# Performance work log

Hardware: AMD Instinct MI355X
Metric: run time of the kernel (lower is better)

## Reference

```python
import jax, jax.numpy as jnp
from jax import lax
import numpy as np

B, N, G, K = 4, 1024, 128, 32
D_MODEL, DEPTH, CLS = 384, 12, 40
D_INNER, D_STATE, D_CONV, DT_RANK = 768, 16, 4, 24
EPS = 1e-5
BN_SCALE = 1.0 / float(np.sqrt(1.0 + EPS))  # eval BN, running_mean=0, running_var=1


def layernorm(x, w, b):
    mu = x.mean(-1, keepdims=True)
    var = ((x - mu) ** 2).mean(-1, keepdims=True)
    return (x - mu) * lax.rsqrt(var + EPS) * w + b


def bn_eval(x, g, b):
    return x * (g * BN_SCALE) + b


def fps(xyz, n):
    Bb, Nn, _ = xyz.shape
    first = jnp.zeros((Bb,), jnp.int32)

    def step(carry, _):
        dmin, last = carry
        p = jnp.take_along_axis(xyz, last[:, None, None], axis=1)  # B,1,3
        dmin = jnp.minimum(dmin, jnp.sum((xyz - p) ** 2, -1))
        nxt = jnp.argmax(dmin, -1).astype(jnp.int32)
        return (dmin, nxt), nxt

    _, rest = lax.scan(step, (jnp.full((Bb, Nn), 1e10, xyz.dtype), first), None, length=n - 1)
    return jnp.concatenate([first[None, :], rest], 0).T  # B,G


def group_points(xyz):
    idx = fps(xyz, G)
    center = jnp.take_along_axis(xyz, idx[:, :, None], axis=1)            # B,G,3
    d2 = jnp.sum((center[:, :, None, :] - xyz[:, None, :, :]) ** 2, -1)   # B,G,N
    _, knn = lax.top_k(-d2, K)                                            # B,G,K
    nb = jax.vmap(lambda p, i: p[i])(xyz, knn)                            # B,G,K,3
    return nb - center[:, :, None, :], center


def encoder(pg, w1, b1, g1, bb1, w2, b2, w3, b3, g2, bb2, w4, b4):
    Bb, Gg, Kk, _ = pg.shape
    f = pg.reshape(Bb * Gg, Kk, 3)
    f = jax.nn.relu(bn_eval(f @ w1.T + b1, g1, bb1))                      # BG,K,128
    f = f @ w2.T + b2                                                     # BG,K,256
    fg = f.max(1, keepdims=True)
    f = jnp.concatenate([jnp.broadcast_to(fg, f.shape), f], -1)           # BG,K,512
    f = jax.nn.relu(bn_eval(f @ w3.T + b3, g2, bb2))
    f = f @ w4.T + b4
    return f.max(1).reshape(Bb, Gg, -1)                                   # B,G,C


def mamba_mixer(x, ipw, cw, cb, xpw, dpw, dpb, A_log, Dp, opw):
    L = x.shape[1]
    xz = x @ ipw.T                                                        # B,L,2*Di
    u, z = jnp.split(xz, 2, -1)
    up = jnp.pad(u, ((0, 0), (D_CONV - 1, 0), (0, 0)))                    # causal depthwise conv
    u = sum(up[:, k:k + L, :] * cw[:, k] for k in range(D_CONV)) + cb
    u = jax.nn.silu(u)
    xdb = u @ xpw.T
    dt, Bm, Cm = jnp.split(xdb, [DT_RANK, DT_RANK + D_STATE], -1)
    dt = jax.nn.softplus(dt @ dpw.T + dpb)                                # B,L,Di
    A = -jnp.exp(A_log)                                                   # Di,Ds

    def step(h, inp):
        dt_t, B_t, C_t, u_t = inp
        h = jnp.exp(dt_t[:, :, None] * A) * h + (dt_t * u_t)[:, :, None] * B_t[:, None, :]
        return h, jnp.einsum('bds,bs->bd', h, C_t)

    h0 = jnp.zeros((x.shape[0], D_INNER, D_STATE), x.dtype)
    _, ys = lax.scan(step, h0, (dt.swapaxes(0, 1), Bm.swapaxes(0, 1), Cm.swapaxes(0, 1), u.swapaxes(0, 1)))
    y = ys.swapaxes(0, 1) + u * Dp
    return (y * jax.nn.silu(z)) @ opw.T


def forward(pts, enc_w1, enc_b1, enc_bn1_g, enc_bn1_b, enc_w2, enc_b2, enc_w3, enc_b3,
            enc_bn2_g, enc_bn2_b, enc_w4, enc_b4, pos_w1, pos_b1, pos_w2, pos_b2,
            ln_w, ln_b, in_proj_w, conv_w, conv_b, x_proj_w, dt_proj_w, dt_proj_b,
            A_log, D_param, out_proj_w, normf_w, normf_b, norm_w, norm_b,
            head_w1, head_b1, head_bn1_g, head_bn1_b, head_w2, head_b2,
            head_bn2_g, head_bn2_b, head_w3, head_b3):
    nb, center = group_points(pts)
    tok = encoder(nb, enc_w1, enc_b1, enc_bn1_g, enc_bn1_b, enc_w2, enc_b2,
                  enc_w3, enc_b3, enc_bn2_g, enc_bn2_b, enc_w4, enc_b4)    # B,G,384
    pos = jax.nn.gelu(center @ pos_w1.T + pos_b1, approximate=False) @ pos_w2.T + pos_b2

    # PointMamba token reordering: sort by center x, y, z and concatenate -> L = 3G
    toks, poss = [], []
    for ax in range(3):
        o = jnp.argsort(center[:, :, ax], axis=-1)[:, :, None]
        toks.append(jnp.take_along_axis(tok, o, axis=1))
        poss.append(jnp.take_along_axis(pos, o, axis=1))
    tok = jnp.concatenate(toks, 1)
    pos = jnp.concatenate(poss, 1)

    h = tok + pos
    res = jnp.zeros_like(h)

    def layer_step(carry, p):
        h, res = carry
        lnw, lnb, ipw, cw, cb, xpw, dpw, dpb, Al, Dp, opw = p
        res = h + res
        x = layernorm(res, lnw, lnb)
        h = mamba_mixer(x, ipw, cw, cb, xpw, dpw, dpb, Al, Dp, opw)
        return (h, res), None

    (h, res), _ = lax.scan(layer_step, (h, res),
                           (ln_w, ln_b, in_proj_w, conv_w, conv_b, x_proj_w,
                            dt_proj_w, dt_proj_b, A_log, D_param, out_proj_w))
    x = layernorm(h + res, normf_w, normf_b)   # MixerModel.norm_f
    x = layernorm(x, norm_w, norm_b)           # PointMamba.norm
    feat = x.mean(1)                           # B,384
    h1 = jax.nn.relu(bn_eval(feat @ head_w1.T + head_b1, head_bn1_g, head_bn1_b))
    h2 = jax.nn.relu(bn_eval(h1 @ head_w2.T + head_b2, head_bn2_g, head_bn2_b))
    return h2 @ head_w3.T + head_b3            # B,CLS


def setup_inputs():
    key = jax.random.key(0)
    ks = iter(jax.random.split(key, 64))

    def rn(shape, s=0.02):
        return jax.random.normal(next(ks), shape, jnp.float32) * s

    inp = dict(
        pts=jax.random.normal(next(ks), (B, N, 3), jnp.float32),
        enc_w1=rn((128, 3), 0.1), enc_b1=jnp.zeros((128,)),
        enc_bn1_g=jnp.ones((128,)), enc_bn1_b=jnp.zeros((128,)),
        enc_w2=rn((256, 128), 0.05), enc_b2=jnp.zeros((256,)),
        enc_w3=rn((512, 512), 0.05), enc_b3=jnp.zeros((512,)),
        enc_bn2_g=jnp.ones((512,)), enc_bn2_b=jnp.zeros((512,)),
        enc_w4=rn((D_MODEL, 512), 0.05), enc_b4=jnp.zeros((D_MODEL,)),
        pos_w1=rn((128, 3), 0.1), pos_b1=jnp.zeros((128,)),
        pos_w2=rn((D_MODEL, 128), 0.05), pos_b2=jnp.zeros((D_MODEL,)),
        ln_w=jnp.ones((DEPTH, D_MODEL)), ln_b=jnp.zeros((DEPTH, D_MODEL)),
        in_proj_w=rn((DEPTH, 2 * D_INNER, D_MODEL)),
        conv_w=rn((DEPTH, D_INNER, D_CONV), 0.2), conv_b=jnp.zeros((DEPTH, D_INNER)),
        x_proj_w=rn((DEPTH, DT_RANK + 2 * D_STATE, D_INNER)),
        dt_proj_w=rn((DEPTH, D_INNER, DT_RANK), 0.1),
        dt_proj_b=jnp.full((DEPTH, D_INNER), -4.6, jnp.float32),
        A_log=jnp.broadcast_to(jnp.log(jnp.arange(1, D_STATE + 1, dtype=jnp.float32)),
                               (DEPTH, D_INNER, D_STATE)).copy(),
        D_param=jnp.ones((DEPTH, D_INNER)),
        out_proj_w=rn((DEPTH, D_MODEL, D_INNER)),
        normf_w=jnp.ones((D_MODEL,)), normf_b=jnp.zeros((D_MODEL,)),
        norm_w=jnp.ones((D_MODEL,)), norm_b=jnp.zeros((D_MODEL,)),
        head_w1=rn((256, D_MODEL), 0.05), head_b1=jnp.zeros((256,)),
        head_bn1_g=jnp.ones((256,)), head_bn1_b=jnp.zeros((256,)),
        head_w2=rn((256, 256), 0.05), head_b2=jnp.zeros((256,)),
        head_bn2_g=jnp.ones((256,)), head_bn2_b=jnp.zeros((256,)),
        head_w3=rn((CLS, 256), 0.05), head_b3=jnp.zeros((CLS,)),
    )
    return inp


def reference(pts, enc_w1, enc_b1, enc_bn1_g, enc_bn1_b, enc_w2, enc_b2, enc_w3, enc_b3,
              enc_bn2_g, enc_bn2_b, enc_w4, enc_b4, pos_w1, pos_b1, pos_w2, pos_b2,
              ln_w, ln_b, in_proj_w, conv_w, conv_b, x_proj_w, dt_proj_w, dt_proj_b,
              A_log, D_param, out_proj_w, normf_w, normf_b, norm_w, norm_b,
              head_w1, head_b1, head_bn1_g, head_bn1_b, head_w2, head_b2,
              head_bn2_g, head_bn2_b, head_w3, head_b3):
    return forward(pts, enc_w1, enc_b1, enc_bn1_g, enc_bn1_b, enc_w2, enc_b2, enc_w3, enc_b3,
                   enc_bn2_g, enc_bn2_b, enc_w4, enc_b4, pos_w1, pos_b1, pos_w2, pos_b2,
                   ln_w, ln_b, in_proj_w, conv_w, conv_b, x_proj_w, dt_proj_w, dt_proj_b,
                   A_log, D_param, out_proj_w, normf_w, normf_b, norm_w, norm_b,
                   head_w1, head_b1, head_bn1_g, head_bn1_b, head_w2, head_b2,
                   head_bn2_g, head_bn2_b, head_w3, head_b3)
```

## Files before the change

### kernel.cpp

```cpp
#include <hip/hip_runtime.h>
#include <hip/hip_bf16.h>

using bf16 = __hip_bfloat16;
using short8  = __attribute__((ext_vector_type(8))) short;
using floatx4 = __attribute__((ext_vector_type(4))) float;
using ull = unsigned long long;

constexpr int Bn = 4, Np = 1024, Gn = 128, Kn = 32;
constexpr int DM = 384, DEPTH = 12, CLSn = 40;
constexpr int DI = 768, DSt = 16, DTR = 24;
constexpr int Ln = 384;
constexpr int NCH = 12, CHS = 32;
constexpr int XDBS = 1536*56;
constexpr float EPSf = 1e-5f;
constexpr float BNS = 0.99999500003749968752f;
constexpr float LOG2E = 1.4426950408889634f;

static __device__ __forceinline__ short f2bf(float f){
  bf16 h = __float2bfloat16(f);
  return *reinterpret_cast<short*>(&h);
}
static __device__ __forceinline__ float fsig(float x){ return 1.f/(1.f + __expf(-x)); }
static __device__ __forceinline__ float fsoftplus(float x){
  return fmaxf(x, 0.f) + __logf(1.f + __expf(-fabsf(x)));
}

template<int CTRL>
static __device__ __forceinline__ int dppmov(int x){
  return __builtin_amdgcn_update_dpp(0, x, CTRL, 0xF, 0xF, true);
}
static __device__ __forceinline__ ull redmax64(ull key){
  #define RSTEP(CTRL) { \
    int hi = (int)(unsigned)(key >> 32), lo = (int)(unsigned)key; \
    int h2 = dppmov<CTRL>(hi), l2 = dppmov<CTRL>(lo); \
    ull k2 = ((ull)(unsigned)h2 << 32) | (unsigned)l2; \
    if (k2 > key) key = k2; }
  RSTEP(0x111) RSTEP(0x112) RSTEP(0x114) RSTEP(0x118) RSTEP(0x142) RSTEP(0x143)
  #undef RSTEP
  return key;
}
static __device__ __forceinline__ int redmax32(int k){
  #define MSTEP(CTRL) { int o = dppmov<CTRL>(k); k = max(k, o); }
  MSTEP(0x111) MSTEP(0x112) MSTEP(0x114) MSTEP(0x118) MSTEP(0x142) MSTEP(0x143)
  #undef MSTEP
  return k;
}

__global__ __launch_bounds__(64) void fps_kernel(const float* __restrict__ pts,
                                                 float* __restrict__ center){
  int b = blockIdx.x, t = threadIdx.x;
  __shared__ float xs[1024], ys[1024], zs[1024];
  const float* p = pts + (size_t)b * Np * 3;
  float X[16], Y[16], Z[16], D[16];
  #pragma unroll
  for (int i = 0; i < 16; ++i){
    int n = t + 64*i;
    float a = p[n*3+0], c = p[n*3+1], e = p[n*3+2];
    X[i] = a; Y[i] = c; Z[i] = e;
    xs[n] = a; ys[n] = c; zs[n] = e;
    D[i] = 1e10f;
  }
  __syncthreads();
  float px = xs[0], py = ys[0], pz = zs[0];
  if (t == 0){
    center[(size_t)(b*Gn)*3+0] = px;
    center[(size_t)(b*Gn)*3+1] = py;
    center[(size_t)(b*Gn)*3+2] = pz;
  }
  for (int it = 1; it < Gn; ++it){
    float dm[16];
    #pragma unroll
    for (int i = 0; i < 16; ++i){
      float dx = __fsub_rn(X[i], px);
      float dy = __fsub_rn(Y[i], py);
      float dz = __fsub_rn(Z[i], pz);
      float d  = __fadd_rn(__fadd_rn(__fmul_rn(dx,dx), __fmul_rn(dy,dy)), __fmul_rn(dz,dz));
      float v  = fminf(D[i], d); D[i] = v; dm[i] = v;
    }
    float m2[8], m4[4];
    #pragma unroll
    for (int i = 0; i < 8; ++i) m2[i] = fmaxf(dm[2*i], dm[2*i+1]);
    #pragma unroll
    for (int i = 0; i < 4; ++i) m4[i] = fmaxf(m2[2*i], m2[2*i+1]);
    float vloc = fmaxf(fmaxf(m4[0], m4[1]), fmaxf(m4[2], m4[3]));
    int kv = redmax32(__float_as_int(vloc));
    float M = __int_as_float(__builtin_amdgcn_readlane(kv, 63));
    int e8[8], e4[4];
    #pragma unroll
    for (int i = 0; i < 8; ++i){
      int ka = (dm[2*i]   == M) ? (2047 - (t + 64*(2*i)))   : 0;
      int kb = (dm[2*i+1] == M) ? (2047 - (t + 64*(2*i+1))) : 0;
      e8[i] = max(ka, kb);
    }
    #pragma unroll
    for (int i = 0; i < 4; ++i) e4[i] = max(e8[2*i], e8[2*i+1]);
    int eloc = max(max(e4[0], e4[1]), max(e4[2], e4[3]));
    eloc = redmax32(eloc);
    int wn = 2047 - __builtin_amdgcn_readlane(eloc, 63);
    wn = min(max(wn, 0), Np-1);
    px = xs[wn]; py = ys[wn]; pz = zs[wn];
    if (t == 0){
      center[(size_t)(b*Gn+it)*3+0] = px;
      center[(size_t)(b*Gn+it)*3+1] = py;
      center[(size_t)(b*Gn+it)*3+2] = pz;
    }
  }
}

__global__ __launch_bounds__(256) void knn_kernel(const float* __restrict__ pts,
                                                  const float* __restrict__ center,
                                                  float* __restrict__ nb){
  int gid = blockIdx.x; int b = gid >> 7;
  __shared__ float d2[1024];
  __shared__ float rv[4]; __shared__ int ri[4];
  int t = threadIdx.x;
  float cx = center[(size_t)gid*3+0], cy = center[(size_t)gid*3+1], cz = center[(size_t)gid*3+2];
  const float* p = pts + (size_t)b * Np * 3;
  for (int n = t; n < Np; n += 256){
    float dx = __fsub_rn(cx, p[n*3+0]);
    float dy = __fsub_rn(cy, p[n*3+1]);
    float dz = __fsub_rn(cz, p[n*3+2]);
    d2[n] = __fadd_rn(__fadd_rn(__fmul_rn(dx,dx), __fmul_rn(dy,dy)), __fmul_rn(dz,dz));
  }
  __syncthreads();
  for (int kk = 0; kk < Kn; ++kk){
    float v = 3e38f; int idx = 0;
    for (int n = t; n < Np; n += 256){
      float d = d2[n];
      if (d < v || (d == v && n < idx)){ v = d; idx = n; }
    }
    ull key = ((ull)(unsigned)(~__float_as_uint(v)) << 32) | (unsigned)(Np-1 - idx);
    key = redmax64(key);
    if ((t & 63) == 63){
      rv[t>>6] = __uint_as_float(~(unsigned)(key >> 32));
      ri[t>>6] = Np-1 - (int)(unsigned)(key & 0xFFFFFFFFu);
    }
    __syncthreads();
    if (t == 0){
      float bv = rv[0]; int bi = ri[0];
      for (int w = 1; w < 4; ++w){
        if (rv[w] < bv || (rv[w] == bv && ri[w] < bi)){ bv = rv[w]; bi = ri[w]; }
      }
      bi = min(max(bi, 0), Np-1);
      nb[((size_t)gid*Kn+kk)*3+0] = __fsub_rn(p[bi*3+0], cx);
      nb[((size_t)gid*Kn+kk)*3+1] = __fsub_rn(p[bi*3+1], cy);
      nb[((size_t)gid*Kn+kk)*3+2] = __fsub_rn(p[bi*3+2], cz);
      d2[bi] = 3e38f;
    }
    __syncthreads();
  }
}

__global__ __launch_bounds__(256) void cvt_all(const float* __restrict__ s0,
    const float* __restrict__ s1, const float* __restrict__ s2,
    const float* __restrict__ s3, const float* __restrict__ s4,
    const float* __restrict__ s5, bf16* __restrict__ dst){
  long i = ((long)blockIdx.x*256 + threadIdx.x)*4;
  if (i >= 11624448L) return;
  const float* s; long off;
  if      (i <  7077888L){ s = s0; off = 0L; }
  else if (i < 10616832L){ s = s1; off =  7077888L; }
  else if (i < 11132928L){ s = s2; off = 10616832L; }
  else if (i < 11165696L){ s = s3; off = 11132928L; }
  else if (i < 11427840L){ s = s4; off = 11165696L; }
  else                   { s = s5; off = 11427840L; }
  float4 v = *(const float4*)(s + (i - off));
  short* o = (short*)dst + i;
  o[0] = f2bf(v.x); o[1] = f2bf(v.y); o[2] = f2bf(v.z); o[3] = f2bf(v.w);
}

template<typename AT, typename WT, int ACT, int MODE>
__global__ __launch_bounds__(256) void gemm_mfma(const AT* __restrict__ A, int lda,
                                                 const WT* __restrict__ W,
                                                 const float* __restrict__ bias,
                                                 const float* __restrict__ gz,
                                                 const float* __restrict__ bbp,
                                                 float* __restrict__ C, int ldc,
                                                 int M, int N, int K){
  __shared__ __align__(16) short As[64*40];
  __shared__ __align__(16) short Ws[64*40];
  int bm = blockIdx.x * 64, bn = blockIdx.y * 64;
  int t = threadIdx.x;
  int row = t >> 2;
  int kseg = (t & 3) * 8;
  int w = t >> 6, lane = t & 63, m16 = lane & 15, q = lane >> 4;
  floatx4 acc[4] = {};
  for (int k0 = 0; k0 < K; k0 += 32){
    {
      const float* Ar = (const float*)A + (size_t)(bm + row)*lda;
      short* dst = &As[row*40 + kseg];
      #pragma unroll
      for (int j = 0; j < 8; ++j){
        int k = k0 + kseg + j;
        dst[j] = (k < K) ? f2bf(Ar[k]) : (short)0;
      }
    }
    {
      int n = bn + row;
      short* dst = &Ws[row*40 + kseg];
      #pragma unroll
      for (int j = 0; j < 8; ++j){
        int k = k0 + kseg + j;
        dst[j] = (n < N && k < K) ? f2bf(((const float*)W)[(size_t)n*K + k]) : (short)0;
      }
    }
    __syncthreads();
    short8 af = *(const short8*)&As[(w*16 + m16)*40 + q*8];
    #pragma unroll
    for (int j = 0; j < 4; ++j){
      short8 bfr = *(const short8*)&Ws[(j*16 + m16)*40 + q*8];
      acc[j] = __builtin_amdgcn_mfma_f32_16x16x32_bf16(af, bfr, acc[j], 0, 0, 0);
    }
    __syncthreads();
  }
  #pragma unroll
  for (int j = 0; j < 4; ++j){
    int n = bn + j*16 + m16;
    if (n < N){
      float bv = bias ? bias[n] : 0.f;
      float gv = 0.f, bbv = 0.f;
      if (ACT == 1){ gv = gz[n] * BNS; bbv = bbp[n]; }
      #pragma unroll
      for (int r = 0; r < 4; ++r){
        int m = bm + w*16 + q*4 + r;
        float v = acc[j][r] + bv;
        if (ACT == 1){ v = v * gv + bbv; v = fmaxf(v, 0.f); }
        C[(size_t)m*ldc + n] = v;
      }
    }
  }
}

template<typename AT, typename WT, int ACT, int MODE>
__global__ __launch_bounds__(256) void gemm_mfma64(const AT* __restrict__ A, int lda,
                                                   const WT* __restrict__ W,
                                                   const float* __restrict__ bias,
                                                   const float* __restrict__ gz,
                                                   const float* __restrict__ bbp,
                                                   float* __restrict__ C, int ldc,
                                                   int M, int N, int K){
  __shared__ __align__(16) short As[64*72];
  __shared__ __align__(16) short Ws[64*72];
  int bm = blockIdx.x * 64, bn = blockIdx.y * 64;
  int t = threadIdx.x;
  int row = t >> 2;
  int kseg = (t & 3) * 16;
  int w = t >> 6, lane = t & 63, m16 = lane & 15, q = lane >> 4;
  floatx4 acc[4] = {};
  for (int k0 = 0; k0 < K; k0 += 64){
    if constexpr (MODE == 1){
      const float* Yr = (const float*)A + (size_t)(bm + row)*lda + k0 + kseg;
      const float* Zr = gz + (size_t)(bm + row)*1536 + 768 + k0 + kseg;
      float y[16], z[16];
      #pragma unroll
      for (int j = 0; j < 4; ++j){
        *(float4*)&y[j*4] = *(const float4*)(Yr + j*4);
        *(float4*)&z[j*4] = *(const float4*)(Zr + j*4);
      }
      short* dst = &As[row*72 + kseg];
      #pragma unroll
      for (int jj = 0; jj < 16; ++jj) dst[jj] = f2bf(y[jj] * (z[jj] * fsig(z[jj])));
    } else if constexpr (sizeof(AT) == 2){
      const short* Ar = (const short*)A + (size_t)(bm + row)*lda + k0 + kseg;
      *(short8*)&As[row*72 + kseg]     = *(const short8*)Ar;
      *(short8*)&As[row*72 + kseg + 8] = *(const short8*)(Ar + 8);
    } else {
      const float* Ar = (const float*)A + (size_t)(bm + row)*lda + k0 + kseg;
      float a[16];
      #pragma unroll
      for (int j = 0; j < 4; ++j) *(float4*)&a[j*4] = *(const float4*)(Ar + j*4);
      short* dst = &As[row*72 + kseg];
      #pragma unroll
      for (int jj = 0; jj < 16; ++jj) dst[jj] = f2bf(a[jj]);
    }
    {
      int n = bn + row;
      if constexpr (sizeof(WT) == 2){
        short8 v0, v1;
        #pragma unroll
        for (int j = 0; j < 8; ++j){ v0[j] = 0; v1[j] = 0; }
        if (n < N){
          const short* Wr = (const short*)W + (size_t)n*K + k0 + kseg;
          v0 = *(const short8*)Wr;
          v1 = *(const short8*)(Wr + 8);
        }
        *(short8*)&Ws[row*72 + kseg]     = v0;
        *(short8*)&Ws[row*72 + kseg + 8] = v1;
      } else {
        short* dst = &Ws[row*72 + kseg];
        if (n < N){
          const float* Wr = (const float*)W + (size_t)n*K + k0 + kseg;
          float wv[16];
          #pragma unroll
          for (int j = 0; j < 4; ++j) *(float4*)&wv[j*4] = *(const float4*)(Wr + j*4);
          #pragma unroll
          for (int jj = 0; jj < 16; ++jj) dst[jj] = f2bf(wv[jj]);
        } else {
          #pragma unroll
          for (int jj = 0; jj < 16; ++jj) dst[jj] = 0;
        }
      }
    }
    __syncthreads();
    short8 af0 = *(const short8*)&As[(w*16 + m16)*72 + q*8];
    short8 af1 = *(const short8*)&As[(w*16 + m16)*72 + 32 + q*8];
    #pragma unroll
    for (int j = 0; j < 4; ++j){
      short8 b0 = *(const short8*)&Ws[(j*16 + m16)*72 + q*8];
      acc[j] = __builtin_amdgcn_mfma_f32_16x16x32_bf16(af0, b0, acc[j], 0, 0, 0);
      short8 b1 = *(const short8*)&Ws[(j*16 + m16)*72 + 32 + q*8];
      acc[j] = __builtin_amdgcn_mfma_f32_16x16x32_bf16(af1, b1, acc[j], 0, 0, 0);
    }
    __syncthreads();
  }
  #pragma unroll
  for (int j = 0; j < 4; ++j){
    int n = bn + j*16 + m16;
    if (n < N){
      float bv = bias ? bias[n] : 0.f;
      float gv = 0.f, bbv = 0.f;
      if (ACT == 1){ gv = gz[n] * BNS; bbv = bbp[n]; }
      #pragma unroll
      for (int r = 0; r < 4; ++r){
        int m = bm + w*16 + q*4 + r;
        float v = acc[j][r] + bv;
        if (ACT == 1){ v = v * gv + bbv; v = fmaxf(v, 0.f); }
        C[(size_t)m*ldc + n] = v;
      }
    }
  }
}

template<typename WT>
__global__ __launch_bounds__(256) void xproj_kernel(const float* __restrict__ xz,
                                                    const WT* __restrict__ W,
                                                    const float* __restrict__ cw,
                                                    const float* __restrict__ cb,
                                                    float* __restrict__ xdbp,
                                                    int KB){
  __shared__ __align__(16) short As[64*72];
  __shared__ __align__(16) short Ws[64*72];
  int bm = blockIdx.x * 64;
  int ks = blockIdx.y;
  int t = threadIdx.x;
  int row = t >> 2, kseg = (t & 3) * 16;
  int w = t >> 6, lane = t & 63, m16 = lane & 15, q = lane >> 4;
  int m = bm + row;
  int l = m % Ln;
  const int kbase = ks * KB;
  floatx4 acc[4] = {};
  const float4 z4 = make_float4(0.f, 0.f, 0.f, 0.f);
  for (int k0 = kbase; k0 < kbase + KB; k0 += 64){
    {
      int ch = k0 + kseg;
      const float* base = xz + (size_t)m*1536 + ch;
      float x0[16], x1[16], x2[16], x3[16];
      #pragma unroll
      for (int j4 = 0; j4 < 4; ++j4){
        *(float4*)&x3[j4*4] = *(const float4*)(base + j4*4);
        *(float4*)&x2[j4*4] = (l >= 1) ? *(const float4*)(base - 1536 + j4*4) : z4;
        *(float4*)&x1[j4*4] = (l >= 2) ? *(const float4*)(base - 2*1536 + j4*4) : z4;
        *(float4*)&x0[j4*4] = (l >= 3) ? *(const float4*)(base - 3*1536 + j4*4) : z4;
      }
      short* dst = &As[row*72 + kseg];
      #pragma unroll
      for (int j = 0; j < 16; ++j){
        float4 wv = *(const float4*)(cw + (size_t)(ch + j)*4);
        float v = x0[j]*wv.x + x1[j]*wv.y + x2[j]*wv.z + x3[j]*wv.w + cb[ch + j];
        v = v * fsig(v);
        dst[j] = f2bf(v);
      }
    }
    {
      int n = row;
      if constexpr (sizeof(WT) == 2){
        short8 v0, v1;
        #pragma unroll
        for (int j = 0; j < 8; ++j){ v0[j] = 0; v1[j] = 0; }
        if (n < 56){
          const short* Wr = (const short*)W + (size_t)n*DI + k0 + kseg;
          v0 = *(const short8*)Wr;
          v1 = *(const short8*)(Wr + 8);
        }
        *(short8*)&Ws[row*72 + kseg]     = v0;
        *(short8*)&Ws[row*72 + kseg + 8] = v1;
      } else {
        short* dst = &Ws[row*72 + kseg];
        if (n < 56){
          const float* Wr = (const float*)W + (size_t)n*DI + k0 + kseg;
          float wv[16];
          #pragma unroll
          for (int j = 0; j < 4; ++j) *(float4*)&wv[j*4] = *(const float4*)(Wr + j*4);
          #pragma unroll
          for (int jj = 0; jj < 16; ++jj) dst[jj] = f2bf(wv[jj]);
        } else {
          #pragma unroll
          for (int jj = 0; jj < 16; ++jj) dst[jj] = 0;
        }
      }
    }
    __syncthreads();
    short8 af0 = *(const short8*)&As[(w*16 + m16)*72 + q*8];
    short8 af1 = *(const short8*)&As[(w*16 + m16)*72 + 32 + q*8];
    #pragma unroll
    for (int j = 0; j < 4; ++j){
      short8 b0 = *(const short8*)&Ws[(j*16 + m16)*72 + q*8];
      acc[j] = __builtin_amdgcn_mfma_f32_16x16x32_bf16(af0, b0, acc[j], 0, 0, 0);
      short8 b1 = *(const short8*)&Ws[(j*16 + m16)*72 + 32 + q*8];
      acc[j] = __builtin_amdgcn_mfma_f32_16x16x32_bf16(af1, b1, acc[j], 0, 0, 0);
    }
    __syncthreads();
  }
  float* C = xdbp + (size_t)ks * XDBS;
  #pragma unroll
  for (int j = 0; j < 4; ++j){
    int n = j*16 + m16;
    if (n < 56){
      #pragma unroll
      for (int r = 0; r < 4; ++r){
        int mm = bm + w*16 + q*4 + r;
        C[(size_t)mm*56 + n] = acc[j][r];
      }
    }
  }
}

__global__ __launch_bounds__(256) void maxk_fg(float* __restrict__ f3in){
  int gg = blockIdx.x; int c = threadIdx.x;
  float m = -3e38f;
  for (int k = 0; k < Kn; ++k) m = fmaxf(m, f3in[((size_t)gg*Kn + k)*512 + 256 + c]);
  for (int k = 0; k < Kn; ++k) f3in[((size_t)gg*Kn + k)*512 + c] = m;
}

__global__ __launch_bounds__(384) void maxk_tok(const float* __restrict__ f4, float* __restrict__ tok){
  int gg = blockIdx.x; int c = threadIdx.x;
  float m = -3e38f;
  for (int k = 0; k < Kn; ++k) m = fmaxf(m, f4[((size_t)gg*Kn + k)*DM + c]);
  tok[(size_t)gg*DM + c] = m;
}

__global__ __launch_bounds__(128) void pos_kernel(const float* __restrict__ center,
                                                  const float* __restrict__ w1, const float* __restrict__ b1,
                                                  const float* __restrict__ w2, const float* __restrict__ b2,
                                                  float* __restrict__ tok){
  int gid = blockIdx.x;
  __shared__ float h1[128]; __shared__ float c3[3];
  int t = threadIdx.x;
  if (t < 3) c3[t] = center[(size_t)gid*3 + t];
  __syncthreads();
  float a = w1[t*3+0]*c3[0] + w1[t*3+1]*c3[1] + w1[t*3+2]*c3[2] + b1[t];
  h1[t] = 0.5f * a * (1.f + erff(a * 0.70710678118654752440f));
  __syncthreads();
  for (int c = t; c < DM; c += 128){
    float s = b2[c];
    for (int j = 0; j < 128; ++j) s += w2[(size_t)c*128 + j] * h1[j];
    tok[(size_t)gid*DM + c] += s;
  }
}

__global__ __launch_bounds__(128) void sort_kernel(const float* __restrict__ center,
                                                   int* __restrict__ order){
  int bax = blockIdx.x; int b = bax / 3, ax = bax % 3;
  __shared__ float key[128];
  int t = threadIdx.x;
  key[t] = center[(size_t)(b*Gn + t)*3 + ax];
  __syncthreads();
  float kt = key[t]; int r = 0;
  for (int j = 0; j < Gn; ++j){
    float kj = key[j];
    r += (kj < kt || (kj == kt && j < t)) ? 1 : 0;
  }
  r = min(max(r, 0), Gn-1);
  order[b*Ln + ax*Gn + r] = t;
}

__global__ __launch_bounds__(256) void build_h(const float* __restrict__ tok,
                        const int* __restrict__ order,
                        float* __restrict__ h, float* __restrict__ res){
  int i = blockIdx.x * blockDim.x + threadIdx.x;
  if (i >= Bn*Ln*DM) return;
  int c = i % DM; int l = (i / DM) % Ln; int b = i / (DM*Ln);
  int src = order[b*Ln + l];
  src = min(max(src, 0), Gn-1);
  h[i] = tok[((size_t)(b*Gn + src))*DM + c];
  res[i] = 0.f;
}

__global__ __launch_bounds__(256) void ln_res_kernel(const float* __restrict__ h,
                                                     float* __restrict__ res,
                                                     bf16* __restrict__ x,
                                                     const float* __restrict__ w,
                                                     const float* __restrict__ bias){
  int wv = threadIdx.x >> 6, ln = threadIdx.x & 63;
  int tokid = blockIdx.x*4 + wv;
  const float* hr = h + (size_t)tokid*DM;
  float* rr = res + (size_t)tokid*DM;
  bf16* xr = x + (size_t)tokid*DM;
  float v[6]; float s = 0.f;
  #pragma unroll
  for (int i = 0; i < 6; ++i){ int c = ln + 64*i; float t = hr[c] + rr[c]; rr[c] = t; v[i] = t; s += t; }
  #pragma unroll
  for (int o = 32; o > 0; o >>= 1) s += __shfl_xor(s, o);
  float mu = s * (1.f/DM);
  float q = 0.f;
  #pragma unroll
  for (int i = 0; i < 6; ++i){ float d = v[i] - mu; q += d*d; }
  #pragma unroll
  for (int o = 32; o > 0; o >>= 1) q += __shfl_xor(q, o);
  float rstd = rsqrtf(q * (1.f/DM) + EPSf);
  #pragma unroll
  for (int i = 0; i < 6; ++i){ int c = ln + 64*i;
    xr[c] = __float2bfloat16((v[i]-mu)*rstd*w[c] + bias[c]); }
}

__global__ __launch_bounds__(256) void scanA_kernel(const float* __restrict__ xz,
                                                    const float* __restrict__ xdbp, int nks,
                                                    const float* __restrict__ cw,
                                                    const float* __restrict__ cb,
                                                    const float* __restrict__ dpw,
                                                    const float* __restrict__ dpb,
                                                    const float* __restrict__ A_log,
                                                    float* __restrict__ SB_S,
                                                    float* __restrict__ SB_dt,
                                                    float* __restrict__ BND){
  __shared__ float sRow[CHS*56];
  __shared__ float sU[CHS*256];
  int blk = blockIdx.x;
  int c = blk % NCH; int bd = blk / NCH; int dch = bd % 3; int b = bd / 3;
  int t = threadIdx.x; int d = dch*256 + t;
  int l0 = c*CHS;
  for (int i = t; i < CHS*56; i += 256){
    size_t base = ((size_t)(b*Ln + l0))*56 + i;
    float s = xdbp[base];
    for (int k = 1; k < nks; ++k) s += xdbp[(size_t)k*XDBS + base];
    sRow[i] = s;
  }
  float xv[CHS+3];
  #pragma unroll
  for (int j = 0; j < 3; ++j){
    int ll = l0 - 3 + j;
    xv[j] = (ll >= 0) ? xz[((size_t)(b*Ln + ll))*1536 + d] : 0.f;
  }
  const float* xp = xz + ((size_t)(b*Ln + l0))*1536 + d;
  #pragma unroll
  for (int i = 0; i < CHS; ++i) xv[3+i] = xp[(size_t)i*1536];
  #pragma unroll
  for (int j = 0; j < 3; ++j) BND[((size_t)blk*3 + j)*256 + t] = xv[j];
  float cw0 = cw[d*4+0], cw1 = cw[d*4+1], cw2 = cw[d*4+2], cw3 = cw[d*4+3];
  float cbv = cb[d];
  #pragma unroll
  for (int i = 0; i < CHS; ++i){
    float v = xv[i]*cw0 + xv[i+1]*cw1 + xv[i+2]*cw2 + xv[i+3]*cw3 + cbv;
    sU[i*256 + t] = v * fsig(v);
  }
  float w[DTR];
  const float* wp = dpw + (size_t)d*DTR;
  #pragma unroll
  for (int j = 0; j < DTR; ++j) w[j] = wp[j];
  float a2[DSt], h[DSt];
  const float* ap = A_log + (size_t)d*DSt;
  #pragma unroll
  for (int s = 0; s < DSt; ++s){ a2[s] = -__expf(ap[s]) * LOG2E; h[s] = 0.f; }
  float dbias = dpb[d];
  float sumdt = 0.f;
  __syncthreads();
  for (int i = 0; i < CHS; ++i){
    int ro = i*56;
    float dtr = dbias;
    #pragma unroll
    for (int j = 0; j < DTR; ++j) dtr += w[j] * sRow[ro + j];
    float dtv = fsoftplus(dtr);
    sumdt += dtv;
    float du = dtv * sU[i*256 + t];
    #pragma unroll
    for (int s = 0; s < DSt; ++s)
      h[s] = exp2f(dtv * a2[s]) * h[s] + du * sRow[ro + 24 + s];
  }
  size_t sb = ((size_t)blk*256 + t)*16;
  #pragma unroll
  for (int s = 0; s < DSt; ++s) SB_S[sb + s] = h[s];
  SB_dt[(size_t)blk*256 + t] = sumdt;
}

__global__ __launch_bounds__(256) void scanB_kernel(float* __restrict__ xz,
                                                    const float* __restrict__ xdbp, int nks,
                                                    const float* __restrict__ cw,
                                                    const float* __restrict__ cb,
                                                    const float* __restrict__ dpw,
                                                    const float* __restrict__ dpb,
                                                    const float* __restrict__ A_log,
                                                    const float* __restrict__ Dp,
                                                    const float* __restrict__ SB_S,
                                                    const float* __restrict__ SB_dt,
                                                    const float* __restrict__ BND){
  __shared__ float sRow[CHS*56];
  __shared__ float sU[CHS*256];
  int blk = blockIdx.x;
  int c = blk % NCH; int bd = blk / NCH; int dch = bd % 3; int b = bd / 3;
  int t = threadIdx.x; int d = dch*256 + t;
  int l0 = c*CHS;
  for (int i = t; i < CHS*56; i += 256){
    size_t base = ((size_t)(b*Ln + l0))*56 + i;
    float s = xdbp[base];
    for (int k = 1; k < nks; ++k) s += xdbp[(size_t)k*XDBS + base];
    sRow[i] = s;
  }
  float xv[CHS+3];
  #pragma unroll
  for (int j = 0; j < 3; ++j) xv[j] = BND[((size_t)blk*3 + j)*256 + t];
  const float* xp = xz + ((size_t)(b*Ln + l0))*1536 + d;
  #pragma unroll
  for (int i = 0; i < CHS; ++i) xv[3+i] = xp[(size_t)i*1536];
  float cw0 = cw[d*4+0], cw1 = cw[d*4+1], cw2 = cw[d*4+2], cw3 = cw[d*4+3];
  float cbv = cb[d];
  #pragma unroll
  for (int i = 0; i < CHS; ++i){
    float v = xv[i]*cw0 + xv[i+1]*cw1 + xv[i+2]*cw2 + xv[i+3]*cw3 + cbv;
    sU[i*256 + t] = v * fsig(v);
  }
  float w[DTR];
  const float* wp = dpw + (size_t)d*DTR;
  #pragma unroll
  for (int j = 0; j < DTR; ++j) w[j] = wp[j];
  float a2[DSt], h[DSt];
  const float* ap = A_log + (size_t)d*DSt;
  #pragma unroll
  for (int s = 0; s < DSt; ++s){ a2[s] = -__expf(ap[s]) * LOG2E; h[s] = 0.f; }
  for (int cc = 0; cc < c; ++cc){
    size_t base = (((size_t)bd*NCH + cc)*256 + t)*16;
    float sd = SB_dt[((size_t)bd*NCH + cc)*256 + t];
    #pragma unroll
    for (int s = 0; s < DSt; ++s)
      h[s] = exp2f(sd * a2[s]) * h[s] + SB_S[base + s];
  }
  float dbias = dpb[d];
  float Dd = Dp[d];
  float* ydst = xz + ((size_t)(b*Ln + l0))*1536 + dch*256;
  __syncthreads();
  for (int i = 0; i < CHS; ++i){
    int ro = i*56;
    float dtr = dbias;
    #pragma unroll
    for (int j = 0; j < DTR; ++j) dtr += w[j] * sRow[ro + j];
    float dtv = fsoftplus(dtr);
    float u = sU[i*256 + t];
    float du = dtv * u;
    float yv = 0.f;
    #pragma unroll
    for (int s = 0; s < DSt; ++s){
      h[s] = exp2f(dtv * a2[s]) * h[s] + du * sRow[ro + 24 + s];
      yv += h[s] * sRow[ro + 40 + s];
    }
    ydst[(size_t)i*1536 + t] = yv + u*Dd;
  }
}

__global__ __launch_bounds__(256) void final_ln_kernel(const float* __restrict__ h,
                                                       const float* __restrict__ res,
                                                       const float* w1, const float* b1,
                                                       const float* w2, const float* b2,
                                                       float* __restrict__ x){
  int wv = threadIdx.x >> 6, ln = threadIdx.x & 63;
  int tokid = blockIdx.x*4 + wv;
  const float* hr = h + (size_t)tokid*DM;
  const float* rr = res + (size_t)tokid*DM;
  float* xr = x + (size_t)tokid*DM;
  float v[6]; float s = 0.f;
  #pragma unroll
  for (int i = 0; i < 6; ++i){ int c = ln + 64*i; v[i] = hr[c] + rr[c]; s += v[i]; }
  #pragma unroll
  for (int o = 32; o > 0; o >>= 1) s += __shfl_xor(s, o);
  float mu = s * (1.f/DM); float q = 0.f;
  #pragma unroll
  for (int i = 0; i < 6; ++i){ float dd = v[i]-mu; q += dd*dd; }
  #pragma unroll
  for (int o = 32; o > 0; o >>= 1) q += __shfl_xor(q, o);
  float rstd = rsqrtf(q * (1.f/DM) + EPSf);
  float u[6]; float s2 = 0.f;
  #pragma unroll
  for (int i = 0; i < 6; ++i){ int c = ln + 64*i; u[i] = (v[i]-mu)*rstd*w1[c] + b1[c]; s2 += u[i]; }
  #pragma unroll
  for (int o = 32; o > 0; o >>= 1) s2 += __shfl_xor(s2, o);
  float mu2 = s2 * (1.f/DM); float q2 = 0.f;
  #pragma unroll
  for (int i = 0; i < 6; ++i){ float dd = u[i]-mu2; q2 += dd*dd; }
  #pragma unroll
  for (int o = 32; o > 0; o >>= 1) q2 += __shfl_xor(q2, o);
  float rstd2 = rsqrtf(q2 * (1.f/DM) + EPSf);
  #pragma unroll
  for (int i = 0; i < 6; ++i){ int c = ln + 64*i; xr[c] = (u[i]-mu2)*rstd2*w2[c] + b2[c]; }
}

__global__ __launch_bounds__(384) void head_kernel(const float* __restrict__ x,
    const float* w1, const float* b1, const float* g1, const float* bb1,
    const float* w2, const float* b2, const float* g2, const float* bb2,
    const float* w3, const float* b3, float* __restrict__ out){
  int b = blockIdx.x; int t = threadIdx.x;
  __shared__ float feat[DM]; __shared__ float h1[256]; __shared__ float h2[256];
  float s = 0.f;
  for (int l = 0; l < Ln; ++l) s += x[((size_t)(b*Ln + l))*DM + t];
  feat[t] = s * (1.f/Ln);
  __syncthreads();
  if (t < 256){
    float a = b1[t];
    for (int j = 0; j < DM; ++j) a += w1[(size_t)t*DM + j] * feat[j];
    a = a * (g1[t] * BNS) + bb1[t];
    h1[t] = fmaxf(a, 0.f);
  }
  __syncthreads();
  if (t < 256){
    float a = b2[t];
    for (int j = 0; j < 256; ++j) a += w2[(size_t)t*256 + j] * h1[j];
    a = a * (g2[t] * BNS) + bb2[t];
    h2[t] = fmaxf(a, 0.f);
  }
  __syncthreads();
  if (t < CLSn){
    float a = b3[t];
    for (int j = 0; j < 256; ++j) a += w3[(size_t)t*256 + j] * h2[j];
    out[b*CLSn + t] = a;
  }
}

extern "C" void kernel_launch(void* const* d_in, const int* in_sizes, int n_in,
                              void* d_out, int out_size, void* d_ws, size_t ws_size,
                              hipStream_t stream) {
  if (n_in < 42) return;
  if (out_size < Bn*CLSn) return;
  constexpr size_t WS_FLOATS = 3919936;
  if (ws_size < WS_FLOATS * sizeof(float)) return;
  constexpr size_t MIDF = 5812224;
  constexpr size_t BIGF = 18874368;
  const bool mid = ws_size >= (WS_FLOATS + MIDF) * sizeof(float);
  const bool big = ws_size >= (WS_FLOATS + MIDF + BIGF) * sizeof(float);

  const float* pts       = (const float*)d_in[0];
  const float* enc_w1    = (const float*)d_in[1];  const float* enc_b1    = (const float*)d_in[2];
  const float* enc_bn1_g = (const float*)d_in[3];  const float* enc_bn1_b = (const float*)d_in[4];
  const float* enc_w2    = (const float*)d_in[5];  const float* enc_b2    = (const float*)d_in[6];
  const float* enc_w3    = (const float*)d_in[7];  const float* enc_b3    = (const float*)d_in[8];
  const float* enc_bn2_g = (const float*)d_in[9];  const float* enc_bn2_b = (const float*)d_in[10];
  const float* enc_w4    = (const float*)d_in[11]; const float* enc_b4    = (const float*)d_in[12];
  const float* pos_w1    = (const float*)d_in[13]; const float* pos_b1    = (const float*)d_in[14];
  const float* pos_w2    = (const float*)d_in[15]; const float* pos_b2    = (const float*)d_in[16];
  const float* ln_w      = (const float*)d_in[17]; const float* ln_b      = (const float*)d_in[18];
  const float* in_proj_w = (const float*)d_in[19];
  const float* conv_w    = (const float*)d_in[20]; const float* conv_b    = (const float*)d_in[21];
  const float* x_proj_w  = (const float*)d_in[22];
  const float* dt_proj_w = (const float*)d_in[23]; const float* dt_proj_b = (const float*)d_in[24];
  const float* A_log     = (const float*)d_in[25]; const float* D_param   = (const float*)d_in[26];
  const float* out_proj_w= (const float*)d_in[27];
  const float* normf_w   = (const float*)d_in[28]; const float* normf_b   = (const float*)d_in[29];
  const float* norm_w    = (const float*)d_in[30]; const float* norm_b    = (const float*)d_in[31];
  const float* head_w1   = (const float*)d_in[32]; const float* head_b1   = (const float*)d_in[33];
  const float* head_bn1_g= (const float*)d_in[34]; const float* head_bn1_b= (const float*)d_in[35];
  const float* head_w2   = (const float*)d_in[36]; const float* head_b2   = (const float*)d_in[37];
  const float* head_bn2_g= (const float*)d_in[38]; const float* head_bn2_b= (const float*)d_in[39];
  const float* head_w3   = (const float*)d_in[40]; const float* head_b3   = (const float*)d_in[41];

  float* ws = (float*)d_ws;
  float* hb   = ws;
  float* resb = ws + 589824;
  float* U    = ws + 1179648;
  float* center = U;
  float* nb     = U + 1536;
  float* tok    = U + 50688;
  int*   order  = (int*)(U + 247296);
  float* eb0    = U + 262144;
  float* eb1    = U + 1310720;
  float* xz   = U;
  float* xdb  = U + 2359296;
  bf16*  xb   = (bf16*)(U + 2445312);
  float* SBdt_s = U + 2445312;
  float* BND  = U + 2482176;
  float* SBS_s  = hb;
  float* xf   = U;
  float* WB = ws + WS_FLOATS;
  bf16* wb_ip = (bf16*)WB;
  bf16* wb_op = (bf16*)(WB + 3538944);
  bf16* wb_xp = (bf16*)(WB + 5308416);
  bf16* wb_e2 = (bf16*)(WB + 5566464);
  bf16* wb_e3 = (bf16*)(WB + 5582848);
  bf16* wb_e4 = (bf16*)(WB + 5713920);
  float* F3in = WB + MIDF;
  float* F3   = WB + MIDF + 8388608;
  float* F1   = WB + MIDF + 16777216;
  float* F4   = F3in;
  float* SBS_b  = F3;
  float* SBdt_b = F1;

  if (mid)
    cvt_all<<<11352, 256, 0, stream>>>(in_proj_w, out_proj_w, x_proj_w,
                                       enc_w2, enc_w3, enc_w4, (bf16*)WB);

  fps_kernel<<<Bn, 64, 0, stream>>>(pts, center);
  knn_kernel<<<Bn*Gn, 256, 0, stream>>>(pts, center, nb);

  if (big){
    gemm_mfma<float,float,1,0><<<dim3(256,2), 256, 0, stream>>>(nb, 3, enc_w1, enc_b1,
        enc_bn1_g, enc_bn1_b, F1, 128, 16384, 128, 3);
    gemm_mfma64<float,bf16,0,0><<<dim3(256,4), 256, 0, stream>>>(F1, 128, wb_e2, enc_b2,
        nullptr, nullptr, F3in + 256, 512, 16384, 256, 128);
    maxk_fg<<<512, 256, 0, stream>>>(F3in);
    gemm_mfma64<float,bf16,1,0><<<dim3(256,8), 256, 0, stream>>>(F3in, 512, wb_e3, enc_b3,
        enc_bn2_g, enc_bn2_b, F3, 512, 16384, 512, 512);
    gemm_mfma64<float,bf16,0,0><<<dim3(256,6), 256, 0, stream>>>(F3, 512, wb_e4, enc_b4,
        nullptr, nullptr, F4, 384, 16384, 384, 512);
    maxk_tok<<<512, 384, 0, stream>>>(F4, tok);
  } else {
    for (int ch = 0; ch < 8; ++ch){
      const float* nb_c = nb + (size_t)ch*2048*3;
      float* tok_c = tok + (size_t)ch*64*DM;
      gemm_mfma<float,float,1,0><<<dim3(32,2), 256, 0, stream>>>(nb_c, 3, enc_w1, enc_b1,
          enc_bn1_g, enc_bn1_b, eb1, 128, 2048, 128, 3);
      if (mid){
        gemm_mfma64<float,bf16,0,0><<<dim3(32,4), 256, 0, stream>>>(eb1, 128, wb_e2, enc_b2,
            nullptr, nullptr, eb0 + 256, 512, 2048, 256, 128);
        maxk_fg<<<64, 256, 0, stream>>>(eb0);
        gemm_mfma64<float,bf16,1,0><<<dim3(32,8), 256, 0, stream>>>(eb0, 512, wb_e3, enc_b3,
            enc_bn2_g, enc_bn2_b, eb1, 512, 2048, 512, 512);
        gemm_mfma64<float,bf16,0,0><<<dim3(32,6), 256, 0, stream>>>(eb1, 512, wb_e4, enc_b4,
            nullptr, nullptr, eb0, 384, 2048, 384, 512);
      } else {
        gemm_mfma64<float,float,0,0><<<dim3(32,4), 256, 0, stream>>>(eb1, 128, enc_w2, enc_b2,
            nullptr, nullptr, eb0 + 256, 512, 2048, 256, 128);
        maxk_fg<<<64, 256, 0, stream>>>(eb0);
        gemm_mfma64<float,float,1,0><<<dim3(32,8), 256, 0, stream>>>(eb0, 512, enc_w3, enc_b3,
            enc_bn2_g, enc_bn2_b, eb1, 512, 2048, 512, 512);
        gemm_mfma64<float,float,0,0><<<dim3(32,6), 256, 0, stream>>>(eb1, 512, enc_w4, enc_b4,
            nullptr, nullptr, eb0, 384, 2048, 384, 512);
      }
      maxk_tok<<<64, 384, 0, stream>>>(eb0, tok_c);
    }
  }

  pos_kernel<<<Bn*Gn, 128, 0, stream>>>(center, pos_w1, pos_b1, pos_w2, pos_b2, tok);
  sort_kernel<<<Bn*3, 128, 0, stream>>>(center, order);
  build_h<<<(Bn*Ln*DM + 255)/256, 256, 0, stream>>>(tok, order, hb, resb);

  const int nks = big ? 4 : 1;
  float* xdbp = big ? F3in : xdb;
  float* SBS  = big ? SBS_b  : SBS_s;
  float* SBdt = big ? SBdt_b : SBdt_s;

  for (int l = 0; l < DEPTH; ++l){
    const float* lnw  = ln_w      + (size_t)l*DM;
    const float* lnb  = ln_b      + (size_t)l*DM;
    const float* ipw  = in_proj_w + (size_t)l*1536*DM;
    const float* cw   = conv_w    + (size_t)l*DI*4;
    const float* cb   = conv_b    + (size_t)l*DI;
    const float* xpw  = x_proj_w  + (size_t)l*56*DI;
    const float* dpw  = dt_proj_w + (size_t)l*DI*DTR;
    const float* dpb  = dt_proj_b + (size_t)l*DI;
    const float* Alg  = A_log     + (size_t)l*DI*DSt;
    const float* Dpar = D_param   + (size_t)l*DI;
    const float* opw  = out_proj_w+ (size_t)l*DM*DI;

    ln_res_kernel<<<Bn*Ln/4, 256, 0, stream>>>(hb, resb, xb, lnw, lnb);
    if (mid){
      gemm_mfma64<bf16,bf16,0,0><<<dim3(24,24), 256, 0, stream>>>(xb, DM,
          wb_ip + (size_t)l*1536*DM, nullptr, nullptr, nullptr, xz, 1536, Bn*Ln, 1536, DM);
    } else {
      gemm_mfma64<bf16,float,0,0><<<dim3(24,24), 256, 0, stream>>>(xb, DM, ipw,
          nullptr, nullptr, nullptr, xz, 1536, Bn*Ln, 1536, DM);
    }
    if (mid)
      xproj_kernel<bf16><<<dim3(24, nks), 256, 0, stream>>>(xz,
          wb_xp + (size_t)l*56*DI, cw, cb, xdbp, DI/nks);
    else
      xproj_kernel<float><<<dim3(24, nks), 256, 0, stream>>>(xz,
          xpw, cw, cb, xdbp, DI/nks);
    scanA_kernel<<<Bn*3*NCH, 256, 0, stream>>>(xz, xdbp, nks, cw, cb,
        dpw, dpb, Alg, SBS, SBdt, BND);
    scanB_kernel<<<Bn*3*NCH, 256, 0, stream>>>(xz, xdbp, nks, cw, cb,
        dpw, dpb, Alg, Dpar, SBS, SBdt, BND);
    if (mid){
      gemm_mfma64<float,bf16,1-1,1><<<dim3(24,6), 256, 0, stream>>>(xz, 1536,
          wb_op + (size_t)l*DM*DI, nullptr, xz, nullptr, hb, DM, Bn*Ln, DM, DI);
    } else {
      gemm_mfma64<float,float,0,1><<<dim3(24,6), 256, 0, stream>>>(xz, 1536, opw,
          nullptr, xz, nullptr, hb, DM, Bn*Ln, DM, DI);
    }
  }

  final_ln_kernel<<<Bn*Ln/4, 256, 0, stream>>>(hb, resb, normf_w, normf_b, norm_w, norm_b, xf);
  head_kernel<<<Bn, 384, 0, stream>>>(xf, head_w1, head_b1, head_bn1_g, head_bn1_b,
                                      head_w2, head_b2, head_bn2_g, head_bn2_b,
                                      head_w3, head_b3, (float*)d_out);
}
```

Before: 1.808 ms.

## Store encoder activations in bf16, fuse gating into scan, widen FPS block

```diff
diff --git a/kernel.cpp b/kernel.cpp
--- a/kernel.cpp
+++ b/kernel.cpp
@@ -39,22 +39,18 @@
   #undef RSTEP
   return key;
 }
-static __device__ __forceinline__ int redmax32(int k){
-  #define MSTEP(CTRL) { int o = dppmov<CTRL>(k); k = max(k, o); }
-  MSTEP(0x111) MSTEP(0x112) MSTEP(0x114) MSTEP(0x118) MSTEP(0x142) MSTEP(0x143)
-  #undef MSTEP
-  return k;
-}
-
-__global__ __launch_bounds__(64) void fps_kernel(const float* __restrict__ pts,
-                                                 float* __restrict__ center){
+
+__global__ __launch_bounds__(256) void fps_kernel(const float* __restrict__ pts,
+                                                  float* __restrict__ center){
   int b = blockIdx.x, t = threadIdx.x;
+  int w = t >> 6, lane = t & 63;
   __shared__ float xs[1024], ys[1024], zs[1024];
+  __shared__ ull red[2][4];
   const float* p = pts + (size_t)b * Np * 3;
-  float X[16], Y[16], Z[16], D[16];
-  #pragma unroll
-  for (int i = 0; i < 16; ++i){
-    int n = t + 64*i;
+  float X[4], Y[4], Z[4], D[4];
+  #pragma unroll
+  for (int i = 0; i < 4; ++i){
+    int n = t + 256*i;
     float a = p[n*3+0], c = p[n*3+1], e = p[n*3+2];
     X[i] = a; Y[i] = c; Z[i] = e;
     xs[n] = a; ys[n] = c; zs[n] = e;
@@ -68,35 +64,24 @@
     center[(size_t)(b*Gn)*3+2] = pz;
   }
   for (int it = 1; it < Gn; ++it){
-    float dm[16];
+    float v = -1.f; int nbest = t;
     #pragma unroll
-    for (int i = 0; i < 16; ++i){
+    for (int i = 0; i < 4; ++i){
       float dx = __fsub_rn(X[i], px);
       float dy = __fsub_rn(Y[i], py);
       float dz = __fsub_rn(Z[i], pz);
       float d  = __fadd_rn(__fadd_rn(__fmul_rn(dx,dx), __fmul_rn(dy,dy)), __fmul_rn(dz,dz));
-      float v  = fminf(D[i], d); D[i] = v; dm[i] = v;
-    }
-    float m2[8], m4[4];
+      float dm = fminf(D[i], d); D[i] = dm;
+      if (dm > v){ v = dm; nbest = t + 256*i; }
+    }
+    ull key = ((ull)__float_as_uint(v) << 32) | (unsigned)(Np-1 - nbest);
+    key = redmax64(key);
+    if (lane == 63) red[it & 1][w] = key;
+    __syncthreads();
+    ull k = red[it & 1][0];
     #pragma unroll
-    for (int i = 0; i < 8; ++i) m2[i] = fmaxf(dm[2*i], dm[2*i+1]);
-    #pragma unroll
-    for (int i = 0; i < 4; ++i) m4[i] = fmaxf(m2[2*i], m2[2*i+1]);
-    float vloc = fmaxf(fmaxf(m4[0], m4[1]), fmaxf(m4[2], m4[3]));
-    int kv = redmax32(__float_as_int(vloc));
-    float M = __int_as_float(__builtin_amdgcn_readlane(kv, 63));
-    int e8[8], e4[4];
-    #pragma unroll
-    for (int i = 0; i < 8; ++i){
-      int ka = (dm[2*i]   == M) ? (2047 - (t + 64*(2*i)))   : 0;
-      int kb = (dm[2*i+1] == M) ? (2047 - (t + 64*(2*i+1))) : 0;
-      e8[i] = max(ka, kb);
-    }
-    #pragma unroll
-    for (int i = 0; i < 4; ++i) e4[i] = max(e8[2*i], e8[2*i+1]);
-    int eloc = max(max(e4[0], e4[1]), max(e4[2], e4[3]));
-    eloc = redmax32(eloc);
-    int wn = 2047 - __builtin_amdgcn_readlane(eloc, 63);
+    for (int j = 1; j < 4; ++j){ ull kj = red[it & 1][j]; if (kj > k) k = kj; }
+    int wn = Np-1 - (int)(unsigned)(k & 0xFFFFFFFFu);
     wn = min(max(wn, 0), Np-1);
     px = xs[wn]; py = ys[wn]; pz = zs[wn];
     if (t == 0){
@@ -169,13 +154,13 @@
   o[0] = f2bf(v.x); o[1] = f2bf(v.y); o[2] = f2bf(v.z); o[3] = f2bf(v.w);
 }
 
-template<typename AT, typename WT, int ACT, int MODE>
+template<typename AT, typename WT, int ACT, int MODE, typename CT = float>
 __global__ __launch_bounds__(256) void gemm_mfma(const AT* __restrict__ A, int lda,
                                                  const WT* __restrict__ W,
                                                  const float* __restrict__ bias,
                                                  const float* __restrict__ gz,
                                                  const float* __restrict__ bbp,
-                                                 float* __restrict__ C, int ldc,
+                                                 CT* __restrict__ C, int ldc,
                                                  int M, int N, int K){
   __shared__ __align__(16) short As[64*40];
   __shared__ __align__(16) short Ws[64*40];
@@ -225,19 +210,20 @@
         int m = bm + w*16 + q*4 + r;
         float v = acc[j][r] + bv;
         if (ACT == 1){ v = v * gv + bbv; v = fmaxf(v, 0.f); }
-        C[(size_t)m*ldc + n] = v;
-      }
-    }
-  }
-}
-
-template<typename AT, typename WT, int ACT, int MODE>
+        if constexpr (sizeof(CT) == 2) C[(size_t)m*ldc + n] = __float2bfloat16(v);
+        else                           C[(size_t)m*ldc + n] = v;
+      }
+    }
+  }
+}
+
+template<typename AT, typename WT, int ACT, int MODE, typename CT = float>
 __global__ __launch_bounds__(256) void gemm_mfma64(const AT* __restrict__ A, int lda,
                                                    const WT* __restrict__ W,
                                                    const float* __restrict__ bias,
                                                    const float* __restrict__ gz,
                                                    const float* __restrict__ bbp,
-                                                   float* __restrict__ C, int ldc,
+                                                   CT* __restrict__ C, int ldc,
                                                    int M, int N, int K){
   __shared__ __align__(16) short As[64*72];
   __shared__ __align__(16) short Ws[64*72];
@@ -325,7 +311,8 @@
         int m = bm + w*16 + q*4 + r;
         float v = acc[j][r] + bv;
         if (ACT == 1){ v = v * gv + bbv; v = fmaxf(v, 0.f); }
-        C[(size_t)m*ldc + n] = v;
+        if constexpr (sizeof(CT) == 2) C[(size_t)m*ldc + n] = __float2bfloat16(v);
+        else                           C[(size_t)m*ldc + n] = v;
       }
     }
   }
@@ -432,6 +419,14 @@
   for (int k = 0; k < Kn; ++k) f3in[((size_t)gg*Kn + k)*512 + c] = m;
 }
 
+__global__ __launch_bounds__(256) void maxk_fg_bf(bf16* __restrict__ f3b){
+  int gg = blockIdx.x; int c = threadIdx.x;
+  float m = -3e38f;
+  for (int k = 0; k < Kn; ++k) m = fmaxf(m, __bfloat162float(f3b[((size_t)gg*Kn + k)*512 + 256 + c]));
+  bf16 mv = __float2bfloat16(m);
+  for (int k = 0; k < Kn; ++k) f3b[((size_t)gg*Kn + k)*512 + c] = mv;
+}
+
 __global__ __launch_bounds__(384) void maxk_tok(const float* __restrict__ f4, float* __restrict__ tok){
   int gg = blockIdx.x; int c = threadIdx.x;
   float m = -3e38f;
@@ -592,7 +587,8 @@
                                                     const float* __restrict__ Dp,
                                                     const float* __restrict__ SB_S,
                                                     const float* __restrict__ SB_dt,
-                                                    const float* __restrict__ BND){
+                                                    const float* __restrict__ BND,
+                                                    bf16* __restrict__ yb){
   __shared__ float sRow[CHS*56];
   __shared__ float sU[CHS*256];
   int blk = blockIdx.x;
@@ -636,6 +632,8 @@
   float dbias = dpb[d];
   float Dd = Dp[d];
   float* ydst = xz + ((size_t)(b*Ln + l0))*1536 + dch*256;
+  const float* zrow = xz + ((size_t)(b*Ln + l0))*1536 + 768 + dch*256;
+  bf16* ybr = yb ? (yb + ((size_t)(b*Ln + l0))*DI + dch*256) : nullptr;
   __syncthreads();
   for (int i = 0; i < CHS; ++i){
     int ro = i*56;
@@ -651,7 +649,13 @@
       h[s] = exp2f(dtv * a2[s]) * h[s] + du * sRow[ro + 24 + s];
       yv += h[s] * sRow[ro + 40 + s];
     }
-    ydst[(size_t)i*1536 + t] = yv + u*Dd;
+    float yfull = yv + u*Dd;
+    if (ybr){
+      float zv = zrow[(size_t)i*1536 + t];
+      ybr[(size_t)i*DI + t] = __float2bfloat16(yfull * (zv * fsig(zv)));
+    } else {
+      ydst[(size_t)i*1536 + t] = yfull;
+    }
   }
 }
 
@@ -782,29 +786,32 @@
   bf16* wb_e2 = (bf16*)(WB + 5566464);
   bf16* wb_e3 = (bf16*)(WB + 5582848);
   bf16* wb_e4 = (bf16*)(WB + 5713920);
-  float* F3in = WB + MIDF;
-  float* F3   = WB + MIDF + 8388608;
-  float* F1   = WB + MIDF + 16777216;
-  float* F4   = F3in;
-  float* SBS_b  = F3;
-  float* SBdt_b = F1;
+  float* BIGB = WB + MIDF;
+  bf16*  F1b  = (bf16*)BIGB;
+  bf16*  F3b  = (bf16*)(BIGB + 1048576);
+  bf16*  F3c  = (bf16*)(BIGB + 5242880);
+  float* F4   = BIGB + 9437184;
+  float* xdbp_b = BIGB + 15728640;
+  float* SBS_b  = BIGB + 16072704;
+  float* SBdt_b = BIGB + 16662528;
+  bf16*  yb     = (bf16*)(BIGB + 16699392);
 
   if (mid)
     cvt_all<<<11352, 256, 0, stream>>>(in_proj_w, out_proj_w, x_proj_w,
                                        enc_w2, enc_w3, enc_w4, (bf16*)WB);
 
-  fps_kernel<<<Bn, 64, 0, stream>>>(pts, center);
+  fps_kernel<<<Bn, 256, 0, stream>>>(pts, center);
   knn_kernel<<<Bn*Gn, 256, 0, stream>>>(pts, center, nb);
 
   if (big){
-    gemm_mfma<float,float,1,0><<<dim3(256,2), 256, 0, stream>>>(nb, 3, enc_w1, enc_b1,
-        enc_bn1_g, enc_bn1_b, F1, 128, 16384, 128, 3);
-    gemm_mfma64<float,bf16,0,0><<<dim3(256,4), 256, 0, stream>>>(F1, 128, wb_e2, enc_b2,
-        nullptr, nullptr, F3in + 256, 512, 16384, 256, 128);
-    maxk_fg<<<512, 256, 0, stream>>>(F3in);
-    gemm_mfma64<float,bf16,1,0><<<dim3(256,8), 256, 0, stream>>>(F3in, 512, wb_e3, enc_b3,
-        enc_bn2_g, enc_bn2_b, F3, 512, 16384, 512, 512);
-    gemm_mfma64<float,bf16,0,0><<<dim3(256,6), 256, 0, stream>>>(F3, 512, wb_e4, enc_b4,
+    gemm_mfma<float,float,1,0,bf16><<<dim3(256,2), 256, 0, stream>>>(nb, 3, enc_w1, enc_b1,
+        enc_bn1_g, enc_bn1_b, F1b, 128, 16384, 128, 3);
+    gemm_mfma64<bf16,bf16,0,0,bf16><<<dim3(256,4), 256, 0, stream>>>(F1b, 128, wb_e2, enc_b2,
+        nullptr, nullptr, F3b + 256, 512, 16384, 256, 128);
+    maxk_fg_bf<<<512, 256, 0, stream>>>(F3b);
+    gemm_mfma64<bf16,bf16,1,0,bf16><<<dim3(256,8), 256, 0, stream>>>(F3b, 512, wb_e3, enc_b3,
+        enc_bn2_g, enc_bn2_b, F3c, 512, 16384, 512, 512);
+    gemm_mfma64<bf16,bf16,0,0,float><<<dim3(256,6), 256, 0, stream>>>(F3c, 512, wb_e4, enc_b4,
         nullptr, nullptr, F4, 384, 16384, 384, 512);
     maxk_tok<<<512, 384, 0, stream>>>(F4, tok);
   } else {
@@ -839,7 +846,7 @@
   build_h<<<(Bn*Ln*DM + 255)/256, 256, 0, stream>>>(tok, order, hb, resb);
 
   const int nks = big ? 4 : 1;
-  float* xdbp = big ? F3in : xdb;
+  float* xdbp = big ? xdbp_b : xdb;
   float* SBS  = big ? SBS_b  : SBS_s;
   float* SBdt = big ? SBdt_b : SBdt_s;
 
@@ -873,9 +880,12 @@
     scanA_kernel<<<Bn*3*NCH, 256, 0, stream>>>(xz, xdbp, nks, cw, cb,
         dpw, dpb, Alg, SBS, SBdt, BND);
     scanB_kernel<<<Bn*3*NCH, 256, 0, stream>>>(xz, xdbp, nks, cw, cb,
-        dpw, dpb, Alg, Dpar, SBS, SBdt, BND);
-    if (mid){
-      gemm_mfma64<float,bf16,1-1,1><<<dim3(24,6), 256, 0, stream>>>(xz, 1536,
+        dpw, dpb, Alg, Dpar, SBS, SBdt, BND, big ? yb : nullptr);
+    if (big){
+      gemm_mfma64<bf16,bf16,0,0><<<dim3(24,6), 256, 0, stream>>>(yb, DI,
+          wb_op + (size_t)l*DM*DI, nullptr, nullptr, nullptr, hb, DM, Bn*Ln, DM, DI);
+    } else if (mid){
+      gemm_mfma64<float,bf16,0,1><<<dim3(24,6), 256, 0, stream>>>(xz, 1536,
           wb_op + (size_t)l*DM*DI, nullptr, xz, nullptr, hb, DM, Bn*Ln, DM, DI);
     } else {
       gemm_mfma64<float,float,0,1><<<dim3(24,6), 256, 0, stream>>>(xz, 1536, opw,
```

New measurement: 1.806 ms. Within noise of the previous version (-0.1%).
